# Kernel tuning notes

Hardware: AMD Instinct MI355X
Metric: run time of the kernel (lower is better)

The kernel has to match this reference:

```python
import jax, jax.numpy as jnp
import numpy as np

N_NODES = 20000
N_EDGES = 320000
DIM_IN = 768
DIM_H = 512
S_HOPS = 3
NUM_GNNS = 4
NEG_SLOPE = 0.2  # DGL GATConv default


def setup_inputs() -> dict:
    key = jax.random.key(0)
    ks = jax.random.split(key, 12)
    feat = jax.random.normal(ks[0], (N_NODES, DIM_IN), dtype=jnp.float32)
    src = jax.random.randint(ks[1], (N_EDGES,), 0, N_NODES)
    dst = jax.random.randint(ks[2], (N_EDGES,), 0, N_NODES)
    # learned params
    fc_W = jax.random.normal(ks[3], (DIM_IN, DIM_H), dtype=jnp.float32) * 0.02
    fc_b = jnp.zeros((DIM_H,), dtype=jnp.float32)
    gat_W = jax.random.normal(ks[4], (NUM_GNNS, DIM_H, DIM_H), dtype=jnp.float32) * 0.02
    gat_al = jax.random.normal(ks[5], (NUM_GNNS, DIM_H), dtype=jnp.float32) * 0.1
    gat_ar = jax.random.normal(ks[6], (NUM_GNNS, DIM_H), dtype=jnp.float32) * 0.1
    gat_b = jnp.zeros((NUM_GNNS, DIM_H), dtype=jnp.float32)
    beta = jnp.ones((S_HOPS + 1,), dtype=jnp.float32)
    return {"feat": feat, "fc_W": fc_W, "fc_b": fc_b, "gat_W": gat_W,
            "gat_al": gat_al, "gat_ar": gat_ar, "gat_b": gat_b,
            "beta": beta, "src": src, "dst": dst}


def _gat_layer(h, W, a_l, a_r, b, src, dst):
    z = h @ W                                   # [N, DH]
    el = z @ a_l                                # [N]
    er = z @ a_r                                # [N]
    e = jax.nn.leaky_relu(el[src] + er[dst], NEG_SLOPE)  # [E]
    # edge softmax over incoming edges of each dst node
    m = jax.ops.segment_max(e, dst, num_segments=N_NODES)
    ex = jnp.exp(e - m[dst])
    denom = jax.ops.segment_sum(ex, dst, num_segments=N_NODES)
    alpha = ex / denom[dst]                     # [E]
    out = jax.ops.segment_sum(alpha[:, None] * z[src], dst, num_segments=N_NODES)
    return out + b


def reference(feat, fc_W, fc_b, gat_W, gat_al, gat_ar, gat_b, beta, src, dst):
    h = feat @ fc_W + fc_b                      # dim_in -> 512
    for l in range(NUM_GNNS):
        h = _gat_layer(h, gat_W[l], gat_al[l], gat_ar[l], gat_b[l], src, dst)
    # A_hat = A + I propagation; A_hat @ Z = scatter(Z[src] -> dst) + Z
    Z_prev = h
    Z = beta[0] * Z_prev                        # accumulated Z is computed but the
    for s in range(1, S_HOPS + 1):              # original module returns Z_prev
        Z_s = jax.ops.segment_sum(Z_prev[src], dst, num_segments=N_NODES) + Z_prev
        Z = Z + beta[s] * Z_s
        Z_prev = Z_s
    return Z_prev
```

## Files before the change

kernel.cpp:

```cpp
#include <hip/hip_runtime.h>
#include <math.h>

#define N_NODES 20000
#define M_PAD   20096
#define N_EDGES 320000
#define DIM_IN 768
#define DIM_H 512
#define NUM_GNNS 4
#define NEG_SLOPE 0.2f

#define GEMM_TILES 628
#define GEMM_GRID  632

#define SLC_GRID 5000

typedef __attribute__((ext_vector_type(8))) short short8;
typedef __attribute__((ext_vector_type(4))) float f32x4;

#define GPTR(p) (const __attribute__((address_space(1))) void*)(p)
#define LPTR(p) (__attribute__((address_space(3))) void*)(p)

__device__ __forceinline__ float bf2f(unsigned int lo16) {
  return __uint_as_float(lo16 << 16);
}
__device__ __forceinline__ unsigned short f2bf(float f) {
  unsigned int u = __float_as_uint(f);
  u += 0x7FFFu + ((u >> 16) & 1u);
  return (unsigned short)(u >> 16);
}
__device__ __forceinline__ void unpack8(uint4 v, float* f) {
  f[0] = bf2f(v.x & 0xffffu); f[1] = bf2f(v.x >> 16);
  f[2] = bf2f(v.y & 0xffffu); f[3] = bf2f(v.y >> 16);
  f[4] = bf2f(v.z & 0xffffu); f[5] = bf2f(v.z >> 16);
  f[6] = bf2f(v.w & 0xffffu); f[7] = bf2f(v.w >> 16);
}
__device__ __forceinline__ uint4 pack8(const float* o) {
  uint4 pv;
  pv.x = (unsigned)f2bf(o[0]) | ((unsigned)f2bf(o[1]) << 16);
  pv.y = (unsigned)f2bf(o[2]) | ((unsigned)f2bf(o[3]) << 16);
  pv.z = (unsigned)f2bf(o[4]) | ((unsigned)f2bf(o[5]) << 16);
  pv.w = (unsigned)f2bf(o[6]) | ((unsigned)f2bf(o[7]) << 16);
  return pv;
}

__device__ __forceinline__ float waveReduceSum(float v) {
#pragma unroll
  for (int off = 32; off > 0; off >>= 1) v += __shfl_xor(v, off, 64);
  return v;
}
__device__ __forceinline__ float waveReduceMax(float v) {
#pragma unroll
  for (int off = 32; off > 0; off >>= 1) v = fmaxf(v, __shfl_xor(v, off, 64));
  return v;
}

__global__ __launch_bounds__(256) void gemm_mfma_bf16(
    const unsigned short* __restrict__ A,
    const unsigned short* __restrict__ Bt,
    const float* __restrict__ bias,
    unsigned short* __restrict__ Cbf,
    int K) {
  int bid = blockIdx.x;
  int tile = (bid & 7) * (GEMM_GRID / 8) + (bid >> 3);
  if (tile >= GEMM_TILES) return;
  int brow = tile >> 2;
  int bcol = tile & 3;

  __shared__ __align__(16) unsigned short lds[4][128 * 32];
  int tid = threadIdx.x;
  int wave = tid >> 6, lane = tid & 63;
  int wm = wave >> 1, wn = wave & 1;

  int rl = lane >> 2;
  int kc = (lane & 3) ^ ((lane >> 3) & 3);
  int r0 = 32 * wave;
  const unsigned short* gA0 = A + (size_t)(brow * 128 + r0 + rl) * K + kc * 8;
  const unsigned short* gA1 = gA0 + (size_t)16 * K;
  const unsigned short* gB0 = Bt + (size_t)(bcol * 128 + r0 + rl) * K + kc * 8;
  const unsigned short* gB1 = gB0 + (size_t)16 * K;

  int mrow = lane & 15;
  int q = lane >> 4;
  int swz = (q ^ ((mrow >> 1) & 3)) * 8;

  f32x4 acc[4][4];
#pragma unroll
  for (int i = 0; i < 4; ++i)
#pragma unroll
    for (int j = 0; j < 4; ++j) acc[i][j] = (f32x4)(0.f);

  int nk = K >> 5;
  {
    unsigned short* lA = lds[0] + r0 * 32;
    unsigned short* lB = lds[2] + r0 * 32;
    __builtin_amdgcn_global_load_lds(GPTR(gA0), LPTR(lA), 16, 0, 0);
    __builtin_amdgcn_global_load_lds(GPTR(gA1), LPTR(lA + 512), 16, 0, 0);
    __builtin_amdgcn_global_load_lds(GPTR(gB0), LPTR(lB), 16, 0, 0);
    __builtin_amdgcn_global_load_lds(GPTR(gB1), LPTR(lB + 512), 16, 0, 0);
  }
  __syncthreads();

  for (int t = 0; t < nk; ++t) {
    int cur = t & 1;
    if (t + 1 < nk) {
      int k0 = (t + 1) << 5;
      unsigned short* lA = lds[cur ^ 1] + r0 * 32;
      unsigned short* lB = lds[2 + (cur ^ 1)] + r0 * 32;
      __builtin_amdgcn_global_load_lds(GPTR(gA0 + k0), LPTR(lA), 16, 0, 0);
      __builtin_amdgcn_global_load_lds(GPTR(gA1 + k0), LPTR(lA + 512), 16, 0, 0);
      __builtin_amdgcn_global_load_lds(GPTR(gB0 + k0), LPTR(lB), 16, 0, 0);
      __builtin_amdgcn_global_load_lds(GPTR(gB1 + k0), LPTR(lB + 512), 16, 0, 0);
    }
    const short8* ra = (const short8*)(lds[cur] + (64 * wm + mrow) * 32 + swz);
    const short8* rb = (const short8*)(lds[2 + cur] + (64 * wn + mrow) * 32 + swz);
    short8 a[4], b[4];
#pragma unroll
    for (int u = 0; u < 4; ++u) a[u] = ra[u * 64];
#pragma unroll
    for (int u = 0; u < 4; ++u) b[u] = rb[u * 64];
#pragma unroll
    for (int mt = 0; mt < 4; ++mt)
#pragma unroll
      for (int nt = 0; nt < 4; ++nt)
        acc[mt][nt] = __builtin_amdgcn_mfma_f32_16x16x32_bf16(a[mt], b[nt], acc[mt][nt], 0, 0, 0);
    __syncthreads();
  }

  unsigned short* Cs = lds[0];
  {
    float bv[4];
#pragma unroll
    for (int nt = 0; nt < 4; ++nt)
      bv[nt] = bias ? bias[bcol * 128 + 64 * wn + 16 * nt + mrow] : 0.f;
#pragma unroll
    for (int mt = 0; mt < 4; ++mt)
#pragma unroll
      for (int nt = 0; nt < 4; ++nt)
#pragma unroll
        for (int i = 0; i < 4; ++i) {
          int row = 64 * wm + 16 * mt + 4 * q + i;
          int col = 64 * wn + 16 * nt + mrow;
          Cs[row * 128 + col] = f2bf(acc[mt][nt][i] + bv[nt]);
        }
  }
  __syncthreads();
  int rr = tid >> 4, cb = (tid & 15) * 8;
#pragma unroll
  for (int it = 0; it < 8; ++it, rr += 16) {
    uint4 val = *(const uint4*)(Cs + rr * 128 + cb);
    *(uint4*)(Cbf + (size_t)(brow * 128 + rr) * DIM_H + bcol * 128 + cb) = val;
  }
}

__global__ void convert_feat(const float* __restrict__ feat, unsigned short* __restrict__ Abf) {
  int t = blockIdx.x * blockDim.x + threadIdx.x;
  const int CHUNKS = M_PAD * DIM_IN / 8;
  if (t >= CHUNKS) return;
  int row = t / (DIM_IN / 8);
  uint4 o;
  if (row < N_NODES) {
    const float4* p = (const float4*)(feat + (size_t)t * 8);
    float4 x = p[0], y = p[1];
    o.x = (unsigned)f2bf(x.x) | ((unsigned)f2bf(x.y) << 16);
    o.y = (unsigned)f2bf(x.z) | ((unsigned)f2bf(x.w) << 16);
    o.z = (unsigned)f2bf(y.x) | ((unsigned)f2bf(y.y) << 16);
    o.w = (unsigned)f2bf(y.z) | ((unsigned)f2bf(y.w) << 16);
  } else {
    o = make_uint4(0, 0, 0, 0);
  }
  ((uint4*)Abf)[t] = o;
}

__global__ __launch_bounds__(256) void transpose_bf16(const float* __restrict__ in,
                                                      unsigned short* __restrict__ out,
                                                      int R, int C) {
  __shared__ float tile[32][33];
  int tx = threadIdx.x, ty = threadIdx.y;
  size_t base = (size_t)blockIdx.z * R * C;
  int r0 = blockIdx.x * 32, c0 = blockIdx.y * 32;
#pragma unroll
  for (int i = 0; i < 4; ++i) {
    int r = r0 + ty + i * 8;
    tile[ty + i * 8][tx] = in[base + (size_t)r * C + c0 + tx];
  }
  __syncthreads();
#pragma unroll
  for (int i = 0; i < 4; ++i) {
    int c = c0 + ty + i * 8;
    out[base + (size_t)c * R + r0 + tx] = f2bf(tile[tx][ty + i * 8]);
  }
}

__global__ void count_edges(const int* __restrict__ dst, int* __restrict__ counts) {
  int k = blockIdx.x * blockDim.x + threadIdx.x;
  if (k < N_EDGES) atomicAdd(&counts[dst[k]], 1);
}

__global__ __launch_bounds__(1024) void scan_kernel(const int* __restrict__ counts,
                                                    int* __restrict__ indptr) {
  __shared__ int part[1024];
  int tid = threadIdx.x;
  const int CH = (N_NODES + 1023) / 1024;
  int base = tid * CH;
  int s = 0;
  for (int i = 0; i < CH; ++i) {
    int idx = base + i;
    if (idx < N_NODES) s += counts[idx];
  }
  part[tid] = s;
  __syncthreads();
  for (int off = 1; off < 1024; off <<= 1) {
    int v = (tid >= off) ? part[tid - off] : 0;
    __syncthreads();
    part[tid] += v;
    __syncthreads();
  }
  int run = (tid == 0) ? 0 : part[tid - 1];
  for (int i = 0; i < CH; ++i) {
    int idx = base + i;
    if (idx < N_NODES) {
      indptr[idx] = run;
      run += counts[idx];
      if (idx == N_NODES - 1) indptr[N_NODES] = run;
    }
  }
}

__global__ void fill_adj(const int* __restrict__ src, const int* __restrict__ dst,
                         const int* __restrict__ indptr, int* __restrict__ cursor,
                         int* __restrict__ adjsrc) {
  int k = blockIdx.x * blockDim.x + threadIdx.x;
  if (k < N_EDGES) {
    int d = dst[k];
    int pos = atomicAdd(&cursor[d], 1);
    adjsrc[indptr[d] + pos] = src[k];
  }
}

__global__ __launch_bounds__(1024) void build_perm(const int* __restrict__ counts,
                                                   int* __restrict__ perm) {
  __shared__ int hist[64];
  __shared__ int basec[64];
  int tid = threadIdx.x;
  if (tid < 64) hist[tid] = 0;
  __syncthreads();
  for (int v = tid; v < N_NODES; v += 1024)
    atomicAdd(&hist[min(counts[v], 63)], 1);
  __syncthreads();
  if (tid == 0) {
    int run = 0;
#pragma unroll
    for (int i = 0; i < 64; ++i) { basec[i] = run; run += hist[i]; }
  }
  __syncthreads();
  for (int v = tid; v < N_NODES; v += 1024) {
    int b = min(counts[v], 63);
    int pos = atomicAdd(&basec[b], 1);
    perm[pos] = v;
  }
}

__global__ __launch_bounds__(256) void eler_bf(const unsigned short* __restrict__ zbf,
                                               const float* __restrict__ al,
                                               const float* __restrict__ ar,
                                               float* __restrict__ el, float* __restrict__ er) {
  int wid = (blockIdx.x * blockDim.x + threadIdx.x) >> 6;
  int lane = threadIdx.x & 63;
  if (wid >= N_NODES) return;
  uint4 zv = ((const uint4*)(zbf + (size_t)wid * DIM_H))[lane];
  float z[8];
  unpack8(zv, z);
  const float4* al4 = (const float4*)(al + lane * 8);
  const float4* ar4 = (const float4*)(ar + lane * 8);
  float4 a0 = al4[0], a1 = al4[1], r0 = ar4[0], r1 = ar4[1];
  float sl = z[0] * a0.x + z[1] * a0.y + z[2] * a0.z + z[3] * a0.w +
             z[4] * a1.x + z[5] * a1.y + z[6] * a1.z + z[7] * a1.w;
  float sr = z[0] * r0.x + z[1] * r0.y + z[2] * r0.z + z[3] * r0.w +
             z[4] * r1.x + z[5] * r1.y + z[6] * r1.z + z[7] * r1.w;
  sl = waveReduceSum(sl);
  sr = waveReduceSum(sr);
  if (lane == 0) { el[wid] = sl; er[wid] = sr; }
}

__global__ __launch_bounds__(256) void edge_softmax_alpha(
    const float* __restrict__ el, const float* __restrict__ er,
    const int* __restrict__ indptr, const int* __restrict__ adjsrc,
    float* __restrict__ alpha, int2* __restrict__ apairs) {
  int v = (blockIdx.x * blockDim.x + threadIdx.x) >> 6;
  int lane = threadIdx.x & 63;
  if (v >= N_NODES) return;
  int begin = indptr[v], end = indptr[v + 1];
  float er_v = er[v];

  float m = -INFINITY;
  for (int j = begin + lane; j < end; j += 64) {
    float e = el[adjsrc[j]] + er_v;
    e = (e >= 0.f) ? e : NEG_SLOPE * e;
    alpha[j] = e;
    m = fmaxf(m, e);
  }
  m = waveReduceMax(m);

  float ss = 0.f;
  for (int j = begin + lane; j < end; j += 64) {
    float ex = __expf(alpha[j] - m);
    alpha[j] = ex;
    ss += ex;
  }
  float denom = waveReduceSum(ss);
  float inv = (end > begin) ? 1.f / denom : 0.f;

  for (int j = begin + lane; j < end; j += 64)
    apairs[j] = make_int2(adjsrc[j], __float_as_int(alpha[j] * inv));
}

__global__ __launch_bounds__(256) void gather_slc(
    const unsigned short* __restrict__ zin, const int2* __restrict__ apairs,
    const int* __restrict__ indptr, const int* __restrict__ adjsrc,
    const int* __restrict__ perm, const float* __restrict__ bias, int self_term,
    unsigned short* __restrict__ out_bf, float* __restrict__ out_f32) {
  int slice = blockIdx.x & 7;
  int grp = blockIdx.x >> 3;
  int wave = threadIdx.x >> 6, lane = threadIdx.x & 63;
  int slot = lane >> 3, sub = lane & 7;
  int vidx = grp * 32 + wave * 8 + slot;
  int v = perm[vidx];
  unsigned cbyte = (unsigned)(slice * 128 + sub * 16);
  const char* zb = (const char*)zin;

  int b = indptr[v];
  unsigned ue = (unsigned)indptr[v + 1];
  int md = (int)ue - b;
  md = max(md, __shfl_xor(md, 8, 64));
  md = max(md, __shfl_xor(md, 16, 64));
  md = max(md, __shfl_xor(md, 32, 64));

  float acc[8];
  if (self_term) {
    uint4 sz = *(const uint4*)(zb + (((unsigned)v) << 10) + cbyte);
    unpack8(sz, acc);
  } else {
#pragma unroll
    for (int i = 0; i < 8; ++i) acc[i] = 0.f;
  }

  unsigned jb = (unsigned)b;
  const unsigned EMAX = (unsigned)(N_EDGES - 1);
  if (apairs) {
    const char* pb = (const char*)apairs;
#pragma nounroll
    for (int t = 0; t < md; t += 8) {
      unsigned j0 = jb + (unsigned)t;
      int idx[8];
      float wv[8];
#pragma unroll
      for (int u = 0; u < 8; ++u) {
        unsigned a = min(j0 + (unsigned)u, EMAX) << 3;
        int2 p = *(const int2*)(pb + a);
        idx[u] = p.x;
        wv[u] = (j0 + (unsigned)u < ue) ? __int_as_float(p.y) : 0.f;
      }
      uint4 z[8];
#pragma unroll
      for (int u = 0; u < 8; ++u)
        z[u] = *(const uint4*)(zb + (((unsigned)idx[u]) << 10) + cbyte);
#pragma unroll
      for (int u = 0; u < 8; ++u) {
        float f[8];
        unpack8(z[u], f);
#pragma unroll
        for (int i = 0; i < 8; ++i) acc[i] = fmaf(wv[u], f[i], acc[i]);
      }
    }
  } else {
    const char* ab = (const char*)adjsrc;
#pragma nounroll
    for (int t = 0; t < md; t += 8) {
      unsigned j0 = jb + (unsigned)t;
      int idx[8];
      float wv[8];
#pragma unroll
      for (int u = 0; u < 8; ++u) {
        unsigned a = min(j0 + (unsigned)u, EMAX) << 2;
        idx[u] = *(const int*)(ab + a);
        wv[u] = (j0 + (unsigned)u < ue) ? 1.f : 0.f;
      }
      uint4 z[8];
#pragma unroll
      for (int u = 0; u < 8; ++u)
        z[u] = *(const uint4*)(zb + (((unsigned)idx[u]) << 10) + cbyte);
#pragma unroll
      for (int u = 0; u < 8; ++u) {
        float f[8];
        unpack8(z[u], f);
#pragma unroll
        for (int i = 0; i < 8; ++i) acc[i] = fmaf(wv[u], f[i], acc[i]);
      }
    }
  }

  if (bias) {
    const float4* b4 = (const float4*)(bias + slice * 64 + sub * 8);
    float4 b0 = b4[0], b1 = b4[1];
    acc[0] += b0.x; acc[1] += b0.y; acc[2] += b0.z; acc[3] += b0.w;
    acc[4] += b1.x; acc[5] += b1.y; acc[6] += b1.z; acc[7] += b1.w;
  }
  if (out_bf) {
    uint4 pv = pack8(acc);
    *(uint4*)((char*)out_bf + (((unsigned)v) << 10) + cbyte) = pv;
  } else {
    char* p = (char*)out_f32 + (((unsigned)v) << 11) + cbyte * 2;
    *(f32x4*)p = (f32x4){acc[0], acc[1], acc[2], acc[3]};
    *(f32x4*)(p + 16) = (f32x4){acc[4], acc[5], acc[6], acc[7]};
  }
}

extern "C" void kernel_launch(void* const* d_in, const int* in_sizes, int n_in,
                              void* d_out, int out_size, void* d_ws, size_t ws_size,
                              hipStream_t stream) {
  const float* feat = (const float*)d_in[0];
  const float* fc_W = (const float*)d_in[1];
  const float* fc_b = (const float*)d_in[2];
  const float* gat_W = (const float*)d_in[3];
  const float* gat_al = (const float*)d_in[4];
  const float* gat_ar = (const float*)d_in[5];
  const float* gat_b = (const float*)d_in[6];
  const int* src = (const int*)d_in[8];
  const int* dst = (const int*)d_in[9];
  float* out = (float*)d_out;

  char* w = (char*)d_ws;
  auto alloc = [&](size_t bytes) {
    char* p = w;
    w += (bytes + 255) & ~(size_t)255;
    return p;
  };
  unsigned short* hbf   = (unsigned short*)alloc((size_t)M_PAD * DIM_H * 2);
  unsigned short* fcWt  = (unsigned short*)alloc((size_t)DIM_H * DIM_IN * 2);
  unsigned short* gatWt = (unsigned short*)alloc((size_t)NUM_GNNS * DIM_H * DIM_H * 2);
  float* el    = (float*)alloc((size_t)N_NODES * 4);
  float* er    = (float*)alloc((size_t)N_NODES * 4);
  int* counts  = (int*)alloc((size_t)2 * N_NODES * 4);
  int* cursor  = counts + N_NODES;
  int* indptr  = (int*)alloc((size_t)(N_NODES + 1) * 4);
  int* adjsrc  = (int*)alloc((size_t)N_EDGES * 4);
  int* perm    = (int*)alloc((size_t)N_NODES * 4);
  char* uni = alloc((size_t)M_PAD * DIM_IN * 2);
  unsigned short* Abf = (unsigned short*)uni;
  float* alpha = (float*)uni;
  int2* apairs = (int2*)(uni + (((size_t)N_EDGES * 4 + 255) & ~(size_t)255));
  unsigned short* Z1  = (unsigned short*)uni;
  unsigned short* zbf = (unsigned short*)d_out;

  hipMemsetAsync(counts, 0, sizeof(int) * 2 * N_NODES, stream);
  count_edges<<<(N_EDGES + 255) / 256, 256, 0, stream>>>(dst, counts);
  scan_kernel<<<1, 1024, 0, stream>>>(counts, indptr);
  fill_adj<<<(N_EDGES + 255) / 256, 256, 0, stream>>>(src, dst, indptr, cursor, adjsrc);
  build_perm<<<1, 1024, 0, stream>>>(counts, perm);

  convert_feat<<<(M_PAD * DIM_IN / 8 + 255) / 256, 256, 0, stream>>>(feat, Abf);
  transpose_bf16<<<dim3(DIM_IN / 32, DIM_H / 32, 1), dim3(32, 8), 0, stream>>>(fc_W, fcWt, DIM_IN, DIM_H);
  transpose_bf16<<<dim3(DIM_H / 32, DIM_H / 32, NUM_GNNS), dim3(32, 8), 0, stream>>>(gat_W, gatWt, DIM_H, DIM_H);

  gemm_mfma_bf16<<<GEMM_GRID, 256, 0, stream>>>(Abf, fcWt, fc_b, hbf, DIM_IN);

  int nwaveblocks = (N_NODES * 64 + 255) / 256;
  for (int l = 0; l < NUM_GNNS; ++l) {
    gemm_mfma_bf16<<<GEMM_GRID, 256, 0, stream>>>(hbf, gatWt + (size_t)l * DIM_H * DIM_H,
                                                  nullptr, zbf, DIM_H);
    eler_bf<<<nwaveblocks, 256, 0, stream>>>(zbf, gat_al + (size_t)l * DIM_H,
                                             gat_ar + (size_t)l * DIM_H, el, er);
    edge_softmax_alpha<<<nwaveblocks, 256, 0, stream>>>(el, er, indptr, adjsrc, alpha, apairs);
    gather_slc<<<SLC_GRID, 256, 0, stream>>>(
        zbf, apairs, indptr, adjsrc, perm, gat_b + (size_t)l * DIM_H, 0, hbf, nullptr);
  }

  gather_slc<<<SLC_GRID, 256, 0, stream>>>(hbf, nullptr, indptr, adjsrc, perm, nullptr, 1, Z1, nullptr);
  gather_slc<<<SLC_GRID, 256, 0, stream>>>(Z1, nullptr, indptr, adjsrc, perm, nullptr, 1, hbf, nullptr);
  gather_slc<<<SLC_GRID, 256, 0, stream>>>(hbf, nullptr, indptr, adjsrc, perm, nullptr, 1, nullptr, out);
}
```

Before: 595.9 us.

## Drop degree-sorted node permutation and prefetch edge pairs in gather loop

Removes the build_perm kernel and degree-bucketed node ordering, so gather_slc processes nodes in natural order. The gather loop is unified into a single apairs path that prefetches the next 8 (index, weight) pairs while the current batch's rows are gathered. Unweighted propagation hops now use apairs filled with weight 1.0 by a new pack_ones kernel. Reads can run past the edge array end, which is masked by clamping node indices and zeroing weights. Dropping the sort risks more load imbalance among the 8 nodes sharing a wave, since the loop runs to the largest degree in the group.

```diff
diff --git a/kernel.cpp b/kernel.cpp
--- a/kernel.cpp
+++ b/kernel.cpp
@@ -237,27 +237,9 @@
   }
 }
 
-__global__ __launch_bounds__(1024) void build_perm(const int* __restrict__ counts,
-                                                   int* __restrict__ perm) {
-  __shared__ int hist[64];
-  __shared__ int basec[64];
-  int tid = threadIdx.x;
-  if (tid < 64) hist[tid] = 0;
-  __syncthreads();
-  for (int v = tid; v < N_NODES; v += 1024)
-    atomicAdd(&hist[min(counts[v], 63)], 1);
-  __syncthreads();
-  if (tid == 0) {
-    int run = 0;
-#pragma unroll
-    for (int i = 0; i < 64; ++i) { basec[i] = run; run += hist[i]; }
-  }
-  __syncthreads();
-  for (int v = tid; v < N_NODES; v += 1024) {
-    int b = min(counts[v], 63);
-    int pos = atomicAdd(&basec[b], 1);
-    perm[pos] = v;
-  }
+__global__ void pack_ones(const int* __restrict__ adjsrc, int2* __restrict__ apairs) {
+  int k = blockIdx.x * blockDim.x + threadIdx.x;
+  if (k < N_EDGES) apairs[k] = make_int2(adjsrc[k], __float_as_int(1.0f));
 }
 
 __global__ __launch_bounds__(256) void eler_bf(const unsigned short* __restrict__ zbf,
@@ -316,21 +298,20 @@
 
 __global__ __launch_bounds__(256) void gather_slc(
     const unsigned short* __restrict__ zin, const int2* __restrict__ apairs,
-    const int* __restrict__ indptr, const int* __restrict__ adjsrc,
-    const int* __restrict__ perm, const float* __restrict__ bias, int self_term,
+    const int* __restrict__ indptr, const float* __restrict__ bias, int self_term,
     unsigned short* __restrict__ out_bf, float* __restrict__ out_f32) {
   int slice = blockIdx.x & 7;
   int grp = blockIdx.x >> 3;
   int wave = threadIdx.x >> 6, lane = threadIdx.x & 63;
   int slot = lane >> 3, sub = lane & 7;
-  int vidx = grp * 32 + wave * 8 + slot;
-  int v = perm[vidx];
+  int v = grp * 32 + wave * 8 + slot;
   unsigned cbyte = (unsigned)(slice * 128 + sub * 16);
   const char* zb = (const char*)zin;
+  const char* pb = (const char*)apairs;
 
   int b = indptr[v];
-  unsigned ue = (unsigned)indptr[v + 1];
-  int md = (int)ue - b;
+  int deg = indptr[v + 1] - b;
+  int md = deg;
   md = max(md, __shfl_xor(md, 8, 64));
   md = max(md, __shfl_xor(md, 16, 64));
   md = max(md, __shfl_xor(md, 32, 64));
@@ -344,59 +325,35 @@
     for (int i = 0; i < 8; ++i) acc[i] = 0.f;
   }
 
-  unsigned jb = (unsigned)b;
-  const unsigned EMAX = (unsigned)(N_EDGES - 1);
-  if (apairs) {
-    const char* pb = (const char*)apairs;
+  const unsigned NMAX = (unsigned)(N_NODES - 1);
+  unsigned ab = ((unsigned)b) << 3;
+  int2 ra[8];
+#pragma unroll
+  for (int u = 0; u < 8; ++u) ra[u] = *(const int2*)(pb + ab + u * 8);
 #pragma nounroll
-    for (int t = 0; t < md; t += 8) {
-      unsigned j0 = jb + (unsigned)t;
-      int idx[8];
-      float wv[8];
-#pragma unroll
-      for (int u = 0; u < 8; ++u) {
-        unsigned a = min(j0 + (unsigned)u, EMAX) << 3;
-        int2 p = *(const int2*)(pb + a);
-        idx[u] = p.x;
-        wv[u] = (j0 + (unsigned)u < ue) ? __int_as_float(p.y) : 0.f;
-      }
-      uint4 z[8];
-#pragma unroll
-      for (int u = 0; u < 8; ++u)
-        z[u] = *(const uint4*)(zb + (((unsigned)idx[u]) << 10) + cbyte);
-#pragma unroll
-      for (int u = 0; u < 8; ++u) {
-        float f[8];
-        unpack8(z[u], f);
-#pragma unroll
-        for (int i = 0; i < 8; ++i) acc[i] = fmaf(wv[u], f[i], acc[i]);
-      }
+  for (int t = 0; t < md; t += 8) {
+    int2 rn[8];
+    if (t + 8 < md) {
+#pragma unroll
+      for (int u = 0; u < 8; ++u) rn[u] = *(const int2*)(pb + ab + 64 + u * 8);
+    } else {
+#pragma unroll
+      for (int u = 0; u < 8; ++u) rn[u] = ra[u];
     }
-  } else {
-    const char* ab = (const char*)adjsrc;
-#pragma nounroll
-    for (int t = 0; t < md; t += 8) {
-      unsigned j0 = jb + (unsigned)t;
-      int idx[8];
-      float wv[8];
-#pragma unroll
-      for (int u = 0; u < 8; ++u) {
-        unsigned a = min(j0 + (unsigned)u, EMAX) << 2;
-        idx[u] = *(const int*)(ab + a);
-        wv[u] = (j0 + (unsigned)u < ue) ? 1.f : 0.f;
-      }
-      uint4 z[8];
-#pragma unroll
-      for (int u = 0; u < 8; ++u)
-        z[u] = *(const uint4*)(zb + (((unsigned)idx[u]) << 10) + cbyte);
-#pragma unroll
-      for (int u = 0; u < 8; ++u) {
-        float f[8];
-        unpack8(z[u], f);
-#pragma unroll
-        for (int i = 0; i < 8; ++i) acc[i] = fmaf(wv[u], f[i], acc[i]);
-      }
+    int rem = deg - t;
+#pragma unroll
+    for (int u = 0; u < 8; ++u) {
+      unsigned uidx = min((unsigned)ra[u].x, NMAX);
+      float wv = (u < rem) ? __int_as_float(ra[u].y) : 0.f;
+      uint4 z = *(const uint4*)(zb + (uidx << 10) + cbyte);
+      float f[8];
+      unpack8(z, f);
+#pragma unroll
+      for (int i = 0; i < 8; ++i) acc[i] = fmaf(wv, f[i], acc[i]);
     }
+#pragma unroll
+    for (int u = 0; u < 8; ++u) ra[u] = rn[u];
+    ab += 64;
   }
 
   if (bias) {
@@ -443,20 +400,18 @@
   int* counts  = (int*)alloc((size_t)2 * N_NODES * 4);
   int* cursor  = counts + N_NODES;
   int* indptr  = (int*)alloc((size_t)(N_NODES + 1) * 4);
-  int* adjsrc  = (int*)alloc((size_t)N_EDGES * 4);
-  int* perm    = (int*)alloc((size_t)N_NODES * 4);
+  int* adjsrc  = (int*)alloc((size_t)(N_EDGES + 64) * 4);
   char* uni = alloc((size_t)M_PAD * DIM_IN * 2);
   unsigned short* Abf = (unsigned short*)uni;
   float* alpha = (float*)uni;
-  int2* apairs = (int2*)(uni + (((size_t)N_EDGES * 4 + 255) & ~(size_t)255));
   unsigned short* Z1  = (unsigned short*)uni;
+  int2* apairs = (int2*)(uni + (size_t)M_PAD * DIM_H * 2);
   unsigned short* zbf = (unsigned short*)d_out;
 
   hipMemsetAsync(counts, 0, sizeof(int) * 2 * N_NODES, stream);
   count_edges<<<(N_EDGES + 255) / 256, 256, 0, stream>>>(dst, counts);
   scan_kernel<<<1, 1024, 0, stream>>>(counts, indptr);
   fill_adj<<<(N_EDGES + 255) / 256, 256, 0, stream>>>(src, dst, indptr, cursor, adjsrc);
-  build_perm<<<1, 1024, 0, stream>>>(counts, perm);
 
   convert_feat<<<(M_PAD * DIM_IN / 8 + 255) / 256, 256, 0, stream>>>(feat, Abf);
   transpose_bf16<<<dim3(DIM_IN / 32, DIM_H / 32, 1), dim3(32, 8), 0, stream>>>(fc_W, fcWt, DIM_IN, DIM_H);
@@ -472,10 +427,11 @@
                                              gat_ar + (size_t)l * DIM_H, el, er);
     edge_softmax_alpha<<<nwaveblocks, 256, 0, stream>>>(el, er, indptr, adjsrc, alpha, apairs);
     gather_slc<<<SLC_GRID, 256, 0, stream>>>(
-        zbf, apairs, indptr, adjsrc, perm, gat_b + (size_t)l * DIM_H, 0, hbf, nullptr);
-  }
-
-  gather_slc<<<SLC_GRID, 256, 0, stream>>>(hbf, nullptr, indptr, adjsrc, perm, nullptr, 1, Z1, nullptr);
-  gather_slc<<<SLC_GRID, 256, 0, stream>>>(Z1, nullptr, indptr, adjsrc, perm, nullptr, 1, hbf, nullptr);
-  gather_slc<<<SLC_GRID, 256, 0, stream>>>(hbf, nullptr, indptr, adjsrc, perm, nullptr, 1, nullptr, out);
-}
+        zbf, apairs, indptr, gat_b + (size_t)l * DIM_H, 0, hbf, nullptr);
+  }
+
+  pack_ones<<<(N_EDGES + 255) / 256, 256, 0, stream>>>(adjsrc, apairs);
+  gather_slc<<<SLC_GRID, 256, 0, stream>>>(hbf, apairs, indptr, nullptr, 1, Z1, nullptr);
+  gather_slc<<<SLC_GRID, 256, 0, stream>>>(Z1, apairs, indptr, nullptr, 1, hbf, nullptr);
+  gather_slc<<<SLC_GRID, 256, 0, stream>>>(hbf, apairs, indptr, nullptr, 1, nullptr, out);
+}
```

Result: faster. 581.7 us (-2.4%).
